# Optimization experiments

Hardware: AMD Instinct MI355X
Metric: run time of the kernel (lower is better)

## Reference

```python
import jax, jax.numpy as jnp
import numpy as np

KSIZE = 3
BJORCK_ITERS = 20
POWER_ITERS = 10


def _power_iteration_sigma(A, u):
    # A: [K, n, n], u: [K, n, 1] -> leading singular value per matrix, [K]
    for _ in range(POWER_ITERS):
        v = jnp.swapaxes(A, -1, -2) @ u
        v = v / jnp.linalg.norm(v, axis=-2, keepdims=True)
        u = A @ v
        u = u / jnp.linalg.norm(u, axis=-2, keepdims=True)
    s = (jnp.swapaxes(u, -1, -2) @ A @ v)[..., 0, 0]
    return s


def _bjorck(w, u):
    # power-iteration scaling is done under no_grad in torch -> stop_gradient
    s = jax.lax.stop_gradient(_power_iteration_sigma(jax.lax.stop_gradient(w), u))
    w = w / s[:, None, None]
    for _ in range(BJORCK_ITERS):
        wtw = jnp.swapaxes(w, -1, -2) @ w
        w = 1.5 * w - 0.5 * (w @ wtw)  # beta = 0.5, first order
    return w


def _block_orth(p1, p2):
    # -> [2, 2, n, n]
    n = p1.shape[0]
    I = jnp.eye(n, dtype=p1.dtype)
    return jnp.stack([
        jnp.stack([p1 @ p2, p1 @ (I - p2)]),
        jnp.stack([(I - p1) @ p2, (I - p1) @ (I - p2)]),
    ])


def _matrix_conv(m1, m2):
    # m1: [k,k,n,n], m2: [l,l,n,n] -> [k+l-1, k+l-1, n, n]
    k, l = m1.shape[0], m2.shape[0]
    size = k + l - 1
    rows = []
    for i in range(size):
        row = []
        for j in range(size):
            acc = 0.0
            for i1 in range(min(k, i + 1)):
                for j1 in range(min(k, j + 1)):
                    if i - i1 < l and j - j1 < l:
                        acc = acc + m1[i1, j1] @ m2[i - i1, j - j1]
            row.append(acc)
        rows.append(jnp.stack(row))
    return jnp.stack(rows)


def _bcop_weight(param_matrices, init_u):
    K, C, _ = param_matrices.shape  # K = 2*(KSIZE-1)+1, C = max_channels
    ortho = _bjorck(param_matrices, init_u)
    H = ortho[0]  # cin == cout == C, full slice
    half = C // 2
    mask = jnp.concatenate(
        [jnp.ones((K - 1, 1, half), ortho.dtype), jnp.zeros((K - 1, 1, C - half), ortho.dtype)],
        axis=-1)
    PQ = ortho[1:] * mask
    PQ = PQ @ jnp.swapaxes(PQ, -1, -2)  # symmetric projections [K-1, C, C]
    p = _block_orth(PQ[0], PQ[1])
    for t in range(1, KSIZE - 1):
        p = _matrix_conv(p, _block_orth(PQ[2 * t], PQ[2 * t + 1]))
    p = jnp.einsum('ab,ijbc->ijac', H, p)  # H @ p[i,j]
    # dict_to_tensor(...).permute(3, 2, 1, 0): [k, k, r, c] -> [c, r, j, i]
    return jnp.transpose(p, (3, 2, 1, 0))  # [C_out, C_in, KSIZE, KSIZE]


def setup_inputs() -> dict:
    key = jax.random.key(0)
    k1, k2, k3, k4 = jax.random.split(key, 4)
    C = 256
    num_kernels = 2 * (KSIZE - 1) + 1
    x = jax.random.normal(k1, (32, C, 64, 64), dtype=jnp.float32)
    param_matrices = jax.random.normal(k2, (num_kernels, C, C), dtype=jnp.float32) / np.sqrt(C)
    init_u = jax.random.normal(k3, (num_kernels, C, 1), dtype=jnp.float32)
    bias = jax.random.uniform(k4, (C,), dtype=jnp.float32, minval=-1.0 / np.sqrt(C), maxval=1.0 / np.sqrt(C))
    return {"x": x, "param_matrices": param_matrices, "init_u": init_u, "bias": bias}


def reference(x, param_matrices, init_u, bias):
    weight = _bcop_weight(param_matrices, init_u)
    # cyclic (circular) padding by k//2 on each side, odd kernel
    pad = KSIZE // 2
    xp = jnp.pad(x, ((0, 0), (0, 0), (pad, pad), (pad, pad)), mode='wrap')
    out = jax.lax.conv_general_dilated(
        xp, weight, window_strides=(1, 1), padding='VALID',
        dimension_numbers=('NCHW', 'OIHW', 'NCHW'))
    return out + bias[None, :, None, None]
```

## Files before the change

kernel.cpp:

```cpp
#include <hip/hip_runtime.h>
#include <stdint.h>

typedef unsigned short u16;
typedef unsigned short u16x4 __attribute__((ext_vector_type(4)));
typedef short bf16x8 __attribute__((ext_vector_type(8)));
typedef float f32x4 __attribute__((ext_vector_type(4)));

#define CDIM 256
#define MSZ 65536

constexpr size_t O_XB   = 0;
constexpr size_t O_AT   = 67108864;
constexpr size_t O_PQH  = 67108864;
constexpr size_t O_PQL  = O_PQH + 524288;
constexpr size_t O_SVAL = 68419584;
constexpr size_t O_W0   = 68419840;
constexpr size_t O_W1   = 71041280;
constexpr size_t O_PH   = 71041280;
constexpr size_t O_PL   = O_PH + 524288;
constexpr size_t O_QTH  = O_PL + 524288;
constexpr size_t O_QTL  = O_QTH + 524288;
constexpr size_t O_TH   = 73662720;
constexpr size_t O_TL   = O_TH + 655360;
constexpr size_t O_RTH  = 74973440;
constexpr size_t O_RTL  = O_RTH + 1179648;
constexpr size_t O_WBQ  = O_RTL + 1179648;

__device__ __forceinline__ u16 f2bf(float f) {
  union { float f; uint32_t u; } a; a.f = f;
  uint32_t u = a.u;
  uint32_t r = u + 0x7FFFu + ((u >> 16) & 1u);
  return (u16)(r >> 16);
}
__device__ __forceinline__ float bf2f(u16 u) {
  union { uint32_t u; float f; } a; a.u = ((uint32_t)u) << 16; return a.f;
}
__device__ __forceinline__ void split_st(u16* hi, u16* lo, float v) {
  u16 h = f2bf(v);
  *hi = h;
  *lo = f2bf(v - bf2f(h));
}
__device__ __forceinline__ void gl16(const void* g, void* l) {
  __builtin_amdgcn_global_load_lds(
      (const __attribute__((address_space(1))) void*)g,
      (__attribute__((address_space(3))) void*)l, 16, 0, 0);
}

__device__ __forceinline__ void cvt_block(const float* __restrict__ x,
                                          u16* __restrict__ xb, int b, char* smem) {
  float (*t)[33] = (float(*)[33])smem;
  int ctile = b & 7, wtile = (b >> 3) & 1, h = (b >> 4) & 63, n = b >> 10;
  int c0 = ctile * 32, w0 = wtile * 32;
  int tid = threadIdx.x;
  #pragma unroll
  for (int p = 0; p < 4; p++) {
    int e = tid + p * 256; int cc = e >> 5, ww = e & 31;
    t[cc][ww] = x[(((size_t)n * 256 + c0 + cc) * 64 + h) * 64 + w0 + ww];
  }
  __syncthreads();
  {
    int ww = tid >> 3, c4 = (tid & 7) * 4;
    u16x4 v;
    #pragma unroll
    for (int j = 0; j < 4; ++j) v[j] = f2bf(t[c4 + j][ww]);
    *(u16x4*)&xb[(((size_t)n * 64 + h) * 64 + w0 + ww) * 256 + c0 + c4] = v;
  }
}

__global__ void wtwA_k(const float* __restrict__ W, float* __restrict__ T) {
  int m = blockIdx.y;
  int i0 = (blockIdx.x >> 3) * 32, j0 = (blockIdx.x & 7) * 32;
  const float* A = W + (size_t)m * MSZ;
  __shared__ float As[32][33], Bs[32][33];
  int tid = threadIdx.x, tx = tid & 15, ty = tid >> 4;
  float a00 = 0, a01 = 0, a10 = 0, a11 = 0;
  for (int kc = 0; kc < CDIM; kc += 32) {
    __syncthreads();
    for (int p = 0; p < 4; p++) {
      int e = tid + p * 256; int kk = e >> 5, cc = e & 31;
      As[kk][cc] = A[(kc + kk) * CDIM + i0 + cc];
      Bs[kk][cc] = A[(kc + kk) * CDIM + j0 + cc];
    }
    __syncthreads();
    #pragma unroll
    for (int kk = 0; kk < 32; kk++) {
      float av0 = As[kk][ty], av1 = As[kk][ty + 16];
      float bv0 = Bs[kk][tx], bv1 = Bs[kk][tx + 16];
      a00 += av0 * bv0; a01 += av0 * bv1; a10 += av1 * bv0; a11 += av1 * bv1;
    }
  }
  float* Tm = T + (size_t)m * MSZ;
  Tm[(i0 + ty) * CDIM + j0 + tx] = a00;
  Tm[(i0 + ty) * CDIM + j0 + tx + 16] = a01;
  Tm[(i0 + ty + 16) * CDIM + j0 + tx] = a10;
  Tm[(i0 + ty + 16) * CDIM + j0 + tx + 16] = a11;
}

__global__ __launch_bounds__(1024) void powerB_k(const float* __restrict__ A,
                                                 const float* __restrict__ B,
                                                 const float* __restrict__ u0,
                                                 float* __restrict__ sval) {
  int m = blockIdx.x;
  int tid = threadIdx.x;
  int t = tid & 255, s = tid >> 8;
  __shared__ float v[256], part[4][257];
  const float* Am = A + (size_t)m * MSZ;
  const float* Bm = B + (size_t)m * MSZ;
  float a = 0.f;
  #pragma unroll 16
  for (int i = 0; i < 64; ++i) a += Am[(s * 64 + i) * 256 + t] * u0[m * 256 + s * 64 + i];
  part[s][t] = a;
  __syncthreads();
  if (s == 0) v[t] = part[0][t] + part[1][t] + part[2][t] + part[3][t];
  __syncthreads();
  for (int it = 0; it < 9; ++it) {
    float b = 0.f;
    #pragma unroll 16
    for (int j = 0; j < 64; ++j) b += Bm[(s * 64 + j) * 256 + t] * v[s * 64 + j];
    part[s][t] = b;
    __syncthreads();
    if (s == 0) v[t] = part[0][t] + part[1][t] + part[2][t] + part[3][t];
    __syncthreads();
  }
  float b = 0.f;
  #pragma unroll 16
  for (int j = 0; j < 64; ++j) b += Bm[(s * 64 + j) * 256 + t] * v[s * 64 + j];
  part[s][t] = b;
  __syncthreads();
  if (s == 0) {
    float w = part[0][t] + part[1][t] + part[2][t] + part[3][t];
    float vv = v[t];
    float d1 = vv * w, d2 = vv * vv;
    for (int off = 32; off; off >>= 1) {
      d1 += __shfl_down(d1, off);
      d2 += __shfl_down(d2, off);
    }
    if ((t & 63) == 0) { part[1][t >> 6] = d1; part[2][t >> 6] = d2; }
  }
  __syncthreads();
  if (tid == 0) {
    float num = part[1][0] + part[1][1] + part[1][2] + part[1][3];
    float den = part[2][0] + part[2][1] + part[2][2] + part[2][3];
    sval[m] = sqrtf(num / den);
  }
}

__global__ void scaleT_k(const float* __restrict__ param, const float* __restrict__ sval,
                         u16* __restrict__ Wh, u16* __restrict__ Wl,
                         u16* __restrict__ Wth, u16* __restrict__ Wtl) {
  __shared__ float tl[32][33];
  int m = blockIdx.y;
  int i0 = (blockIdx.x >> 3) * 32, j0 = (blockIdx.x & 7) * 32;
  int tid = threadIdx.x;
  float inv = 1.0f / sval[m];
  const float* Am = param + (size_t)m * MSZ;
  size_t mo = (size_t)m * MSZ;
  for (int p = 0; p < 4; ++p) {
    int e = tid + p * 256; int ii = e >> 5, jj = e & 31;
    float v = Am[(i0 + ii) * 256 + j0 + jj] * inv;
    tl[ii][jj] = v;
    size_t idx = mo + (size_t)(i0 + ii) * 256 + j0 + jj;
    split_st(&Wh[idx], &Wl[idx], v);
  }
  __syncthreads();
  for (int p = 0; p < 4; ++p) {
    int e = tid + p * 256; int jj = e >> 5, ii = e & 31;
    float v = tl[ii][jj];
    size_t idxT = mo + (size_t)(j0 + jj) * 256 + i0 + ii;
    split_st(&Wth[idxT], &Wtl[idxT], v);
  }
}

__device__ __forceinline__ void gemm32_acc(
    const u16* __restrict__ Ah, const u16* __restrict__ Al, int i0,
    const u16* __restrict__ Bh, const u16* __restrict__ Bl, int j0,
    int K, f32x4* acc, char* smem, int tid)
{
  int lane = tid & 63, wave = tid >> 6;
  int qm = wave >> 1, qn = wave & 1;
  int ra = qm * 16 + (lane & 15);
  int rb = qn * 16 + (lane & 15);
  int kb = (lane >> 4) * 16;
  for (int kc = 0; kc < K; kc += 128) {
    __syncthreads();
    #pragma unroll
    for (int p = 0; p < 8; ++p) {
      int e = tid + p * 256;
      int bufi = e >> 9;
      int r = (e >> 4) & 31;
      int cb = (e & 15) * 16;
      const u16* srcm = (bufi == 0) ? Ah : (bufi == 1) ? Al : (bufi == 2) ? Bh : Bl;
      int r0 = (bufi < 2) ? i0 : j0;
      const char* src = (const char*)srcm + ((size_t)(r0 + r) * 256 + kc) * 2 + cb;
      *(uint4*)(smem + bufi * 8192 + r * 256 + (cb ^ ((r & 7) << 4))) = *(const uint4*)src;
    }
    __syncthreads();
    #pragma unroll
    for (int ks = 0; ks < 4; ++ks) {
      int kbyte = ks * 64 + kb;
      int oa = ra * 256 + (kbyte ^ ((ra & 7) << 4));
      int ob = rb * 256 + (kbyte ^ ((rb & 7) << 4));
      bf16x8 ah = *(const bf16x8*)(smem + oa);
      bf16x8 al = *(const bf16x8*)(smem + 8192 + oa);
      bf16x8 bh = *(const bf16x8*)(smem + 16384 + ob);
      bf16x8 bl = *(const bf16x8*)(smem + 24576 + ob);
      *acc = __builtin_amdgcn_mfma_f32_16x16x32_bf16(ah, bh, *acc, 0, 0, 0);
      *acc = __builtin_amdgcn_mfma_f32_16x16x32_bf16(ah, bl, *acc, 0, 0, 0);
      *acc = __builtin_amdgcn_mfma_f32_16x16x32_bf16(al, bh, *acc, 0, 0, 0);
    }
  }
}

#define GEMM_IDX \
  int tid = threadIdx.x; \
  int lane = tid & 63, wave = tid >> 6, qm = wave >> 1, qn = wave & 1; \
  int orow = qm * 16 + ((lane >> 4) << 2); \
  int ocol = qn * 16 + (lane & 15); \
  int i0 = (blockIdx.x >> 3) * 32, j0 = (blockIdx.x & 7) * 32; \
  __shared__ char smem[32768];

__global__ __launch_bounds__(256) void bjorck_t_k(
    const u16* __restrict__ Wth, const u16* __restrict__ Wtl,
    u16* __restrict__ Th, u16* __restrict__ Tl,
    const float* __restrict__ x, u16* __restrict__ xb, int cvt_base) {
  __shared__ char smem[32768];
  int bx = blockIdx.x;
  if (bx >= 320) {
    int b = cvt_base + bx - 320;
    if (b < 32768) cvt_block(x, xb, b, smem);
    return;
  }
  int tid = threadIdx.x;
  int lane = tid & 63, wave = tid >> 6, qm = wave >> 1, qn = wave & 1;
  int orow = qm * 16 + ((lane >> 4) << 2);
  int ocol = qn * 16 + (lane & 15);
  int i0 = ((bx & 63) >> 3) * 32, j0 = (bx & 7) * 32;
  size_t mo = (size_t)(bx >> 6) * MSZ;
  f32x4 acc = {};
  gemm32_acc(Wth + mo, Wtl + mo, i0, Wth + mo, Wtl + mo, j0, 256, &acc, smem, tid);
  #pragma unroll
  for (int v = 0; v < 4; ++v) {
    size_t idx = mo + (size_t)(i0 + orow + v) * 256 + (j0 + ocol);
    split_st(&Th[idx], &Tl[idx], acc[v]);
  }
}

__global__ __launch_bounds__(256) void bjorck_u_k(
    const u16* __restrict__ Wh, const u16* __restrict__ Wl,
    const u16* __restrict__ Th, const u16* __restrict__ Tl,
    u16* __restrict__ nWh, u16* __restrict__ nWl,
    u16* __restrict__ nWth, u16* __restrict__ nWtl,
    const float* __restrict__ x, u16* __restrict__ xb, int cvt_base) {
  __shared__ char smem[32768];
  int bx = blockIdx.x;
  if (bx >= 320) {
    int b = cvt_base + bx - 320;
    if (b < 32768) cvt_block(x, xb, b, smem);
    return;
  }
  int tid = threadIdx.x;
  int lane = tid & 63, wave = tid >> 6, qm = wave >> 1, qn = wave & 1;
  int orow = qm * 16 + ((lane >> 4) << 2);
  int ocol = qn * 16 + (lane & 15);
  int i0 = ((bx & 63) >> 3) * 32, j0 = (bx & 7) * 32;
  size_t mo = (size_t)(bx >> 6) * MSZ;
  f32x4 acc = {};
  gemm32_acc(Wh + mo, Wl + mo, i0, Th + mo, Tl + mo, j0, 256, &acc, smem, tid);
  #pragma unroll
  for (int v = 0; v < 4; ++v) {
    int r = i0 + orow + v, c = j0 + ocol;
    size_t idx = mo + (size_t)r * 256 + c;
    float wv = bf2f(Wh[idx]) + bf2f(Wl[idx]);
    float nv = 1.5f * wv - 0.5f * acc[v];
    split_st(&nWh[idx], &nWl[idx], nv);
    size_t idxT = mo + (size_t)c * 256 + r;
    split_st(&nWth[idxT], &nWtl[idxT], nv);
  }
}

__global__ __launch_bounds__(256) void pq_k(
    const u16* __restrict__ Wh, const u16* __restrict__ Wl,
    u16* __restrict__ PQh, u16* __restrict__ PQl) {
  GEMM_IDX
  int m4 = blockIdx.y;
  const u16* Oh = Wh + (size_t)(1 + m4) * MSZ;
  const u16* Ol = Wl + (size_t)(1 + m4) * MSZ;
  f32x4 acc = {};
  gemm32_acc(Oh, Ol, i0, Oh, Ol, j0, 128, &acc, smem, tid);
  #pragma unroll
  for (int v = 0; v < 4; ++v) {
    size_t idx = (size_t)m4 * MSZ + (size_t)(i0 + orow + v) * 256 + (j0 + ocol);
    split_st(&PQh[idx], &PQl[idx], acc[v]);
  }
}

__global__ __launch_bounds__(256) void c12b_k(
    const u16* __restrict__ PQh, const u16* __restrict__ PQl,
    u16* __restrict__ Ph, u16* __restrict__ Pl,
    u16* __restrict__ QTh, u16* __restrict__ QTl) {
  GEMM_IDX
  f32x4 a1 = {}, a2t = {};
  gemm32_acc(PQh, PQl, i0, PQh + MSZ, PQl + MSZ, j0, 256, &a1, smem, tid);
  gemm32_acc(PQh + 3 * MSZ, PQl + 3 * MSZ, i0, PQh + 2 * MSZ, PQl + 2 * MSZ, j0,
             256, &a2t, smem, tid);
  #pragma unroll
  for (int v = 0; v < 4; ++v) {
    int row = i0 + orow + v, col = j0 + ocol;
    size_t g = (size_t)row * 256 + col;
    float I = (row == col) ? 1.f : 0.f;
    float p0 = bf2f(PQh[g]) + bf2f(PQl[g]);
    float p1 = bf2f(PQh[MSZ + g]) + bf2f(PQl[MSZ + g]);
    float c1 = a1[v];
    split_st(&Ph[g],           &Pl[g],           c1);
    split_st(&Ph[MSZ + g],     &Pl[MSZ + g],     p0 - c1);
    split_st(&Ph[2*MSZ + g],   &Pl[2*MSZ + g],   p1 - c1);
    split_st(&Ph[3*MSZ + g],   &Pl[3*MSZ + g],   I - p0 - p1 + c1);
    float q0 = bf2f(PQh[2*MSZ + g]) + bf2f(PQl[2*MSZ + g]);
    float q1 = bf2f(PQh[3*MSZ + g]) + bf2f(PQl[3*MSZ + g]);
    float c2t = a2t[v];
    split_st(&QTh[g],          &QTl[g],          c2t);
    split_st(&QTh[MSZ + g],    &QTl[MSZ + g],    q0 - c2t);
    split_st(&QTh[2*MSZ + g],  &QTl[2*MSZ + g],  q1 - c2t);
    split_st(&QTh[3*MSZ + g],  &QTl[3*MSZ + g],  I - q0 - q1 + c2t);
  }
}

__global__ __launch_bounds__(256) void mconv_k(
    const u16* __restrict__ Ph, const u16* __restrict__ Pl,
    const u16* __restrict__ QTh, const u16* __restrict__ QTl,
    u16* __restrict__ RTh, u16* __restrict__ RTl) {
  GEMM_IDX
  int ij = blockIdx.y;
  const int toff[10] = {0, 1, 3, 4, 6, 10, 12, 13, 15, 16};
  const int tp[16] = {0, 0, 1, 1, 0, 2, 0, 1, 2, 3, 1, 3, 2, 2, 3, 3};
  const int tq[16] = {0, 1, 0, 1, 2, 0, 3, 2, 1, 0, 3, 1, 2, 3, 2, 3};
  f32x4 acc = {};
  for (int t = toff[ij]; t < toff[ij + 1]; ++t) {
    gemm32_acc(Ph + (size_t)tp[t] * MSZ, Pl + (size_t)tp[t] * MSZ, i0,
               QTh + (size_t)tq[t] * MSZ, QTl + (size_t)tq[t] * MSZ, j0, 256, &acc, smem, tid);
  }
  #pragma unroll
  for (int v = 0; v < 4; ++v) {
    int r = i0 + orow + v, c = j0 + ocol;
    size_t idxT = (size_t)ij * MSZ + (size_t)c * 256 + r;
    split_st(&RTh[idxT], &RTl[idxT], acc[v]);
  }
}

__global__ __launch_bounds__(256) void final_k(
    const u16* __restrict__ Hh, const u16* __restrict__ Hl,
    const u16* __restrict__ RTh, const u16* __restrict__ RTl,
    u16* __restrict__ WBQ) {
  GEMM_IDX
  int ij = blockIdx.y;
  f32x4 acc = {};
  gemm32_acc(Hh, Hl, i0, RTh + (size_t)ij * MSZ, RTl + (size_t)ij * MSZ, j0,
             256, &acc, smem, tid);
  #pragma unroll
  for (int v = 0; v < 4; ++v) {
    int r = i0 + orow + v, c = j0 + ocol;
    int ct = r >> 6, ks = (r >> 5) & 1, jj = (r >> 3) & 3, e = r & 7;
    int s = jj ^ ((c >> 1) & 3);
    int g = ct * 18 + ij * 2 + ks;
    WBQ[(size_t)g * 8192 + (size_t)(c * 4 + s) * 8 + e] = f2bf(acc[v]);
  }
}

__global__ __launch_bounds__(256, 2) void conv_k(
    const u16* __restrict__ xb, const u16* __restrict__ Wb,
    const float* __restrict__ bias, float* __restrict__ out) {
  int braw = blockIdx.x;
  int L = (braw & 7) * 128 + (braw >> 3);
  int h2 = L & 31, n = L >> 5;
  int h0 = h2 * 2;
  int tid = threadIdx.x;
  int lane = tid & 63, wave = tid >> 6;
  int wm = wave >> 1, wn = wave & 1;
  int fr = lane & 15, q = lane >> 4;

  __shared__ char smem[65536];
  char* sX = smem;
  char* sW = smem + 32768;

  f32x4 acc[4][8] = {};

  auto issueX = [&](int ct) {
    #pragma unroll
    for (int i = 0; i < 8; ++i) {
      int d = (wave * 8 + i) * 64 + lane;
      int cb = (d & 7) * 16;
      int w = (d >> 3) & 63;
      int r = d >> 9;
      int hs = (h0 - 1 + r) & 63;
      const char* src = (const char*)xb + (((size_t)(n * 64 + hs) * 64 + w) << 9)
                        + ct * 128 + (cb ^ ((w & 7) << 4));
      gl16(src, sX + (wave * 8 + i) * 1024);
    }
  };
  auto issueW = [&](int g) {
    const char* base = (const char*)Wb + (size_t)g * 16384;
    char* dst = sW + (g & 1) * 16384;
    #pragma unroll
    for (int i = 0; i < 4; ++i) {
      int c = (wave * 4 + i) * 64 + lane;
      gl16(base + c * 16, dst + (wave * 4 + i) * 1024);
    }
  };

  issueX(0);
  issueW(0);
  __syncthreads();

  for (int g = 0; g < 72; ++g) {
    int ct = g / 18, r18 = g % 18, tap = r18 >> 1, ks = r18 & 1;
    int kh = tap % 3, kw = tap / 3;
    if (g + 1 < 72) issueW(g + 1);
    const char* wb = sW + (g & 1) * 16384;
    __builtin_amdgcn_s_setprio(1);
    {
      bf16x8 af[4], bfr[8];
      #pragma unroll
      for (int fn = 0; fn < 8; ++fn) {
        int cl = wn * 128 + fn * 16 + fr;
        bfr[fn] = *(const bf16x8*)(wb + cl * 64 + ((q ^ ((cl >> 1) & 3)) << 4));
      }
      int kb2 = ks * 64 + q * 16;
      #pragma unroll
      for (int fm = 0; fm < 4; ++fm) {
        int wsrc = (fm * 16 + fr + kw + 63) & 63;
        af[fm] = *(const bf16x8*)(sX + ((wm + kh) * 64 + wsrc) * 128 + (kb2 ^ ((wsrc & 7) << 4)));
      }
      #pragma unroll
      for (int fm = 0; fm < 4; ++fm)
        #pragma unroll
        for (int fn = 0; fn < 8; ++fn)
          acc[fm][fn] = __builtin_amdgcn_mfma_f32_16x16x32_bf16(af[fm], bfr[fn], acc[fm][fn], 0, 0, 0);
    }
    __builtin_amdgcn_s_setprio(0);
    if (r18 == 17 && ct < 3) {
      __syncthreads();
      issueX(ct + 1);
      __syncthreads();
    } else {
      __syncthreads();
    }
  }

  __syncthreads();
  float* sF = (float*)smem;
  #pragma unroll
  for (int r = 0; r < 2; ++r) {
    if (wn == r) {
      #pragma unroll
      for (int fn = 0; fn < 8; ++fn) {
        int cl = fn * 16 + fr;
        float bv = bias[r * 128 + cl];
        #pragma unroll
        for (int fm = 0; fm < 4; ++fm) {
          f32x4 v = acc[fm][fn];
          v[0] += bv; v[1] += bv; v[2] += bv; v[3] += bv;
          *(f32x4*)((char*)sF + cl * 512 + wm * 256 +
                    (((unsigned)(fm * 64 + q * 16)) ^ ((unsigned)(cl & 7) << 4))) = v;
        }
      }
    }
    __syncthreads();
    #pragma unroll
    for (int p = 0; p < 16; ++p) {
      int e = tid + p * 256;
      int w4 = e & 15, hloc = (e >> 4) & 1, cl = e >> 5;
      f32x4 val = *(const f32x4*)((const char*)sF + cl * 512 + hloc * 256 +
                                  (((unsigned)(w4 * 16)) ^ ((unsigned)(cl & 7) << 4)));
      *(f32x4*)(out + (((size_t)n * 256 + r * 128 + cl) * 64 + (h0 + hloc)) * 64 + w4 * 4) = val;
    }
    if (r == 0) __syncthreads();
  }
}

extern "C" void kernel_launch(void* const* d_in, const int* in_sizes, int n_in,
                              void* d_out, int out_size, void* d_ws, size_t ws_size,
                              hipStream_t stream) {
  const float* x = (const float*)d_in[0];
  const float* param = (const float*)d_in[1];
  const float* u0 = (const float*)d_in[2];
  const float* bias = (const float*)d_in[3];
  float* out = (float*)d_out;
  char* ws = (char*)d_ws;
  (void)in_sizes; (void)n_in; (void)out_size; (void)ws_size;

  float* B = (float*)(ws + O_AT);
  float* sval = (float*)(ws + O_SVAL);
  u16* xb = (u16*)(ws + O_XB);
  u16* W0h  = (u16*)(ws + O_W0);   u16* W0l  = W0h + 327680;
  u16* W0th = W0l + 327680;        u16* W0tl = W0th + 327680;
  u16* W1h  = (u16*)(ws + O_W1);   u16* W1l  = W1h + 327680;
  u16* W1th = W1l + 327680;        u16* W1tl = W1th + 327680;
  u16* Th = (u16*)(ws + O_TH);     u16* Tl = (u16*)(ws + O_TL);
  u16* PQh = (u16*)(ws + O_PQH);   u16* PQl = (u16*)(ws + O_PQL);
  u16* Ph = (u16*)(ws + O_PH);     u16* Pl = (u16*)(ws + O_PL);
  u16* QTh = (u16*)(ws + O_QTH);   u16* QTl = (u16*)(ws + O_QTL);
  u16* RTh = (u16*)(ws + O_RTH);   u16* RTl = (u16*)(ws + O_RTL);
  u16* WBQ = (u16*)(ws + O_WBQ);

  wtwA_k<<<dim3(64, 5), 256, 0, stream>>>(param, B);
  powerB_k<<<5, 1024, 0, stream>>>(param, B, u0, sval);
  scaleT_k<<<dim3(64, 5), 256, 0, stream>>>(param, sval, W0h, W0l, W0th, W0tl);

  u16 *cWh = W0h, *cWl = W0l, *cWth = W0th, *cWtl = W0tl;
  u16 *nWh = W1h, *nWl = W1l, *nWth = W1th, *nWtl = W1tl;
  for (int it = 0; it < 20; ++it) {
    bjorck_t_k<<<1140, 256, 0, stream>>>(cWth, cWtl, Th, Tl,
                                         x, xb, (2 * it) * 820);
    bjorck_u_k<<<1140, 256, 0, stream>>>(cWh, cWl, Th, Tl, nWh, nWl, nWth, nWtl,
                                         x, xb, (2 * it + 1) * 820);
    u16* t0;
    t0 = cWh; cWh = nWh; nWh = t0;
    t0 = cWl; cWl = nWl; nWl = t0;
    t0 = cWth; cWth = nWth; nWth = t0;
    t0 = cWtl; cWtl = nWtl; nWtl = t0;
  }

  pq_k<<<dim3(64, 4), 256, 0, stream>>>(cWh, cWl, PQh, PQl);
  c12b_k<<<64, 256, 0, stream>>>(PQh, PQl, Ph, Pl, QTh, QTl);
  mconv_k<<<dim3(64, 9), 256, 0, stream>>>(Ph, Pl, QTh, QTl, RTh, RTl);
  final_k<<<dim3(64, 9), 256, 0, stream>>>(cWh, cWl, RTh, RTl, WBQ);

  conv_k<<<1024, 256, 0, stream>>>(xb, WBQ, bias, out);
}
```

Before: 444.7 us.

## Use single-bf16 GEMMs for early Bjorck iterations and reuse precomputed WtW

```diff
diff --git a/kernel.cpp b/kernel.cpp
--- a/kernel.cpp
+++ b/kernel.cpp
@@ -145,22 +145,27 @@
   }
 }
 
-__global__ void scaleT_k(const float* __restrict__ param, const float* __restrict__ sval,
+__global__ void scaleT_k(const float* __restrict__ param, const float* __restrict__ B,
+                         const float* __restrict__ sval,
                          u16* __restrict__ Wh, u16* __restrict__ Wl,
-                         u16* __restrict__ Wth, u16* __restrict__ Wtl) {
+                         u16* __restrict__ Wth, u16* __restrict__ Wtl,
+                         u16* __restrict__ Th, u16* __restrict__ Tl) {
   __shared__ float tl[32][33];
   int m = blockIdx.y;
   int i0 = (blockIdx.x >> 3) * 32, j0 = (blockIdx.x & 7) * 32;
   int tid = threadIdx.x;
   float inv = 1.0f / sval[m];
+  float inv2 = inv * inv;
   const float* Am = param + (size_t)m * MSZ;
+  const float* Bm = B + (size_t)m * MSZ;
   size_t mo = (size_t)m * MSZ;
   for (int p = 0; p < 4; ++p) {
     int e = tid + p * 256; int ii = e >> 5, jj = e & 31;
-    float v = Am[(i0 + ii) * 256 + j0 + jj] * inv;
+    size_t rel = (size_t)(i0 + ii) * 256 + j0 + jj;
+    float v = Am[rel] * inv;
     tl[ii][jj] = v;
-    size_t idx = mo + (size_t)(i0 + ii) * 256 + j0 + jj;
-    split_st(&Wh[idx], &Wl[idx], v);
+    split_st(&Wh[mo + rel], &Wl[mo + rel], v);
+    split_st(&Th[mo + rel], &Tl[mo + rel], Bm[rel] * inv2);
   }
   __syncthreads();
   for (int p = 0; p < 4; ++p) {
@@ -171,6 +176,7 @@
   }
 }
 
+template<bool FULL>
 __device__ __forceinline__ void gemm32_acc(
     const u16* __restrict__ Ah, const u16* __restrict__ Al, int i0,
     const u16* __restrict__ Bh, const u16* __restrict__ Bl, int j0,
@@ -183,16 +189,30 @@
   int kb = (lane >> 4) * 16;
   for (int kc = 0; kc < K; kc += 128) {
     __syncthreads();
-    #pragma unroll
-    for (int p = 0; p < 8; ++p) {
-      int e = tid + p * 256;
-      int bufi = e >> 9;
-      int r = (e >> 4) & 31;
-      int cb = (e & 15) * 16;
-      const u16* srcm = (bufi == 0) ? Ah : (bufi == 1) ? Al : (bufi == 2) ? Bh : Bl;
-      int r0 = (bufi < 2) ? i0 : j0;
-      const char* src = (const char*)srcm + ((size_t)(r0 + r) * 256 + kc) * 2 + cb;
-      *(uint4*)(smem + bufi * 8192 + r * 256 + (cb ^ ((r & 7) << 4))) = *(const uint4*)src;
+    if (FULL) {
+      #pragma unroll
+      for (int p = 0; p < 8; ++p) {
+        int e = tid + p * 256;
+        int bufi = e >> 9;
+        int r = (e >> 4) & 31;
+        int cb = (e & 15) * 16;
+        const u16* srcm = (bufi == 0) ? Ah : (bufi == 1) ? Al : (bufi == 2) ? Bh : Bl;
+        int r0 = (bufi < 2) ? i0 : j0;
+        const char* src = (const char*)srcm + ((size_t)(r0 + r) * 256 + kc) * 2 + cb;
+        *(uint4*)(smem + bufi * 8192 + r * 256 + (cb ^ ((r & 7) << 4))) = *(const uint4*)src;
+      }
+    } else {
+      #pragma unroll
+      for (int p = 0; p < 4; ++p) {
+        int e = tid + p * 256;
+        int which = e >> 9;
+        int r = (e >> 4) & 31;
+        int cb = (e & 15) * 16;
+        const u16* srcm = which ? Bh : Ah;
+        int r0 = which ? j0 : i0;
+        const char* src = (const char*)srcm + ((size_t)(r0 + r) * 256 + kc) * 2 + cb;
+        *(uint4*)(smem + which * 16384 + r * 256 + (cb ^ ((r & 7) << 4))) = *(const uint4*)src;
+      }
     }
     __syncthreads();
     #pragma unroll
@@ -201,12 +221,14 @@
       int oa = ra * 256 + (kbyte ^ ((ra & 7) << 4));
       int ob = rb * 256 + (kbyte ^ ((rb & 7) << 4));
       bf16x8 ah = *(const bf16x8*)(smem + oa);
-      bf16x8 al = *(const bf16x8*)(smem + 8192 + oa);
       bf16x8 bh = *(const bf16x8*)(smem + 16384 + ob);
-      bf16x8 bl = *(const bf16x8*)(smem + 24576 + ob);
       *acc = __builtin_amdgcn_mfma_f32_16x16x32_bf16(ah, bh, *acc, 0, 0, 0);
-      *acc = __builtin_amdgcn_mfma_f32_16x16x32_bf16(ah, bl, *acc, 0, 0, 0);
-      *acc = __builtin_amdgcn_mfma_f32_16x16x32_bf16(al, bh, *acc, 0, 0, 0);
+      if (FULL) {
+        bf16x8 al = *(const bf16x8*)(smem + 8192 + oa);
+        bf16x8 bl = *(const bf16x8*)(smem + 24576 + ob);
+        *acc = __builtin_amdgcn_mfma_f32_16x16x32_bf16(ah, bl, *acc, 0, 0, 0);
+        *acc = __builtin_amdgcn_mfma_f32_16x16x32_bf16(al, bh, *acc, 0, 0, 0);
+      }
     }
   }
 }
@@ -219,6 +241,7 @@
   int i0 = (blockIdx.x >> 3) * 32, j0 = (blockIdx.x & 7) * 32; \
   __shared__ char smem[32768];
 
+template<bool FULL>
 __global__ __launch_bounds__(256) void bjorck_t_k(
     const u16* __restrict__ Wth, const u16* __restrict__ Wtl,
     u16* __restrict__ Th, u16* __restrict__ Tl,
@@ -237,7 +260,7 @@
   int i0 = ((bx & 63) >> 3) * 32, j0 = (bx & 7) * 32;
   size_t mo = (size_t)(bx >> 6) * MSZ;
   f32x4 acc = {};
-  gemm32_acc(Wth + mo, Wtl + mo, i0, Wth + mo, Wtl + mo, j0, 256, &acc, smem, tid);
+  gemm32_acc<FULL>(Wth + mo, Wtl + mo, i0, Wth + mo, Wtl + mo, j0, 256, &acc, smem, tid);
   #pragma unroll
   for (int v = 0; v < 4; ++v) {
     size_t idx = mo + (size_t)(i0 + orow + v) * 256 + (j0 + ocol);
@@ -245,6 +268,7 @@
   }
 }
 
+template<bool FULL>
 __global__ __launch_bounds__(256) void bjorck_u_k(
     const u16* __restrict__ Wh, const u16* __restrict__ Wl,
     const u16* __restrict__ Th, const u16* __restrict__ Tl,
@@ -265,7 +289,7 @@
   int i0 = ((bx & 63) >> 3) * 32, j0 = (bx & 7) * 32;
   size_t mo = (size_t)(bx >> 6) * MSZ;
   f32x4 acc = {};
-  gemm32_acc(Wh + mo, Wl + mo, i0, Th + mo, Tl + mo, j0, 256, &acc, smem, tid);
+  gemm32_acc<FULL>(Wh + mo, Wl + mo, i0, Th + mo, Tl + mo, j0, 256, &acc, smem, tid);
   #pragma unroll
   for (int v = 0; v < 4; ++v) {
     int r = i0 + orow + v, c = j0 + ocol;
@@ -286,7 +310,7 @@
   const u16* Oh = Wh + (size_t)(1 + m4) * MSZ;
   const u16* Ol = Wl + (size_t)(1 + m4) * MSZ;
   f32x4 acc = {};
-  gemm32_acc(Oh, Ol, i0, Oh, Ol, j0, 128, &acc, smem, tid);
+  gemm32_acc<true>(Oh, Ol, i0, Oh, Ol, j0, 128, &acc, smem, tid);
   #pragma unroll
   for (int v = 0; v < 4; ++v) {
     size_t idx = (size_t)m4 * MSZ + (size_t)(i0 + orow + v) * 256 + (j0 + ocol);
@@ -300,9 +324,9 @@
     u16* __restrict__ QTh, u16* __restrict__ QTl) {
   GEMM_IDX
   f32x4 a1 = {}, a2t = {};
-  gemm32_acc(PQh, PQl, i0, PQh + MSZ, PQl + MSZ, j0, 256, &a1, smem, tid);
-  gemm32_acc(PQh + 3 * MSZ, PQl + 3 * MSZ, i0, PQh + 2 * MSZ, PQl + 2 * MSZ, j0,
-             256, &a2t, smem, tid);
+  gemm32_acc<true>(PQh, PQl, i0, PQh + MSZ, PQl + MSZ, j0, 256, &a1, smem, tid);
+  gemm32_acc<true>(PQh + 3 * MSZ, PQl + 3 * MSZ, i0, PQh + 2 * MSZ, PQl + 2 * MSZ, j0,
+                   256, &a2t, smem, tid);
   #pragma unroll
   for (int v = 0; v < 4; ++v) {
     int row = i0 + orow + v, col = j0 + ocol;
@@ -336,8 +360,8 @@
   const int tq[16] = {0, 1, 0, 1, 2, 0, 3, 2, 1, 0, 3, 1, 2, 3, 2, 3};
   f32x4 acc = {};
   for (int t = toff[ij]; t < toff[ij + 1]; ++t) {
-    gemm32_acc(Ph + (size_t)tp[t] * MSZ, Pl + (size_t)tp[t] * MSZ, i0,
-               QTh + (size_t)tq[t] * MSZ, QTl + (size_t)tq[t] * MSZ, j0, 256, &acc, smem, tid);
+    gemm32_acc<true>(Ph + (size_t)tp[t] * MSZ, Pl + (size_t)tp[t] * MSZ, i0,
+                     QTh + (size_t)tq[t] * MSZ, QTl + (size_t)tq[t] * MSZ, j0, 256, &acc, smem, tid);
   }
   #pragma unroll
   for (int v = 0; v < 4; ++v) {
@@ -354,8 +378,8 @@
   GEMM_IDX
   int ij = blockIdx.y;
   f32x4 acc = {};
-  gemm32_acc(Hh, Hl, i0, RTh + (size_t)ij * MSZ, RTl + (size_t)ij * MSZ, j0,
-             256, &acc, smem, tid);
+  gemm32_acc<true>(Hh, Hl, i0, RTh + (size_t)ij * MSZ, RTl + (size_t)ij * MSZ, j0,
+                   256, &acc, smem, tid);
   #pragma unroll
   for (int v = 0; v < 4; ++v) {
     int r = i0 + orow + v, c = j0 + ocol;
@@ -504,15 +528,29 @@
 
   wtwA_k<<<dim3(64, 5), 256, 0, stream>>>(param, B);
   powerB_k<<<5, 1024, 0, stream>>>(param, B, u0, sval);
-  scaleT_k<<<dim3(64, 5), 256, 0, stream>>>(param, sval, W0h, W0l, W0th, W0tl);
+  scaleT_k<<<dim3(64, 5), 256, 0, stream>>>(param, B, sval, W0h, W0l, W0th, W0tl, Th, Tl);
 
   u16 *cWh = W0h, *cWl = W0l, *cWth = W0th, *cWtl = W0tl;
   u16 *nWh = W1h, *nWl = W1l, *nWth = W1th, *nWtl = W1tl;
+  int lc = 0;
+  const int CVT = 841;
   for (int it = 0; it < 20; ++it) {
-    bjorck_t_k<<<1140, 256, 0, stream>>>(cWth, cWtl, Th, Tl,
-                                         x, xb, (2 * it) * 820);
-    bjorck_u_k<<<1140, 256, 0, stream>>>(cWh, cWl, Th, Tl, nWh, nWl, nWth, nWtl,
-                                         x, xb, (2 * it + 1) * 820);
+    if (it > 0) {
+      if (it < 14)
+        bjorck_t_k<false><<<320 + CVT, 256, 0, stream>>>(cWth, cWtl, Th, Tl,
+                                                         x, xb, (lc++) * CVT);
+      else
+        bjorck_t_k<true><<<320 + CVT, 256, 0, stream>>>(cWth, cWtl, Th, Tl,
+                                                        x, xb, (lc++) * CVT);
+    }
+    if (it < 14)
+      bjorck_u_k<false><<<320 + CVT, 256, 0, stream>>>(cWh, cWl, Th, Tl,
+                                                       nWh, nWl, nWth, nWtl,
+                                                       x, xb, (lc++) * CVT);
+    else
+      bjorck_u_k<true><<<320 + CVT, 256, 0, stream>>>(cWh, cWl, Th, Tl,
+                                                      nWh, nWl, nWth, nWtl,
+                                                      x, xb, (lc++) * CVT);
     u16* t0;
     t0 = cWh; cWh = nWh; nWh = t0;
     t0 = cWl; cWl = nWl; nWl = t0;
```

After: 431.0 us. 3.1% less time.
